# Kernel tuning notes

Hardware: AMD Instinct MI355X
Metric: run time of the kernel (lower is better)

Reference implementation:

```python
import jax, jax.numpy as jnp
import numpy as np

SCENE = (128, 128, 8)      # (X, Y, Z) voxel grid
VOXEL_SIZE = 0.4
DOWNSAMPLE_Z = 2
NUM_HEADS = 8
NUM_POINTS = 4
LN_EPS = 1e-5


def _pix2vox(depth, K, E, voxel_origin):
    # depth [1,H,W]; K [1,3,3]; E [1,4,4]; voxel_origin [1,3]
    B, H, W = depth.shape
    gx, gy = jnp.meshgrid(jnp.arange(W, dtype=depth.dtype), jnp.arange(H, dtype=depth.dtype))
    pix = jnp.stack([gx, gy])                              # [2,H,W] -> (u, v) after flip in torch
    d = depth[:, None]                                     # [B,1,H,W]
    p_x = jnp.concatenate([pix[None] * d, d], 1).reshape(B, 3, -1)
    p_c = jnp.linalg.inv(K) @ p_x                          # camera coords [B,3,HW]
    p_c = jnp.concatenate([p_c, jnp.ones_like(p_c[:, :1])], 1)
    p_w = jnp.linalg.inv(E) @ p_c                          # world coords [B,4,HW]
    p_v = (jnp.swapaxes(p_w[:, :3], 1, 2) - voxel_origin[:, None, :]) / VOXEL_SIZE - 0.5
    p_v = p_v.at[..., 2].set(p_v[..., 2] / DOWNSAMPLE_Z)
    return jnp.trunc(p_v).astype(jnp.int32)               # torch .long() truncates toward 0


def _voxel_mask(p_v):
    X, Y, Z = SCENE
    p = p_v[0]                                             # [HW,3] (batch asserted == 1)
    valid = ((p[:, 0] >= 0) & (p[:, 0] < X) & (p[:, 1] >= 0) & (p[:, 1] < Y)
             & (p[:, 2] >= 0) & (p[:, 2] < Z))
    flat = jnp.where(valid, (p[:, 0] * Y + p[:, 1]) * Z + p[:, 2], 0)
    return jnp.zeros(X * Y * Z, dtype=bool).at[flat].max(valid)


def _ms_deform_attn(q, feats, ref, Wv, bv, Woff, boff, Wattw, battw, Wout, bout):
    # q [N,C]; feats: list of [C,Hl,Wl]; ref [N,2] normalized (shared across levels)
    N, C = q.shape
    hd = C // NUM_HEADS
    shapes = [(f.shape[1], f.shape[2]) for f in feats]
    L = len(feats)
    flat = jnp.concatenate([f.reshape(C, -1).T for f in feats], 0)      # [Lsum, C]
    value = (flat @ Wv.T + bv).reshape(-1, NUM_HEADS, hd)               # [Lsum, h, hd]
    off = (q @ Woff.T + boff).reshape(N, NUM_HEADS, L, NUM_POINTS, 2)
    w = jax.nn.softmax((q @ Wattw.T + battw).reshape(N, NUM_HEADS, L * NUM_POINTS), -1)
    w = w.reshape(N, NUM_HEADS, L, NUM_POINTS)
    normalizer = jnp.array([[wl, hl] for (hl, wl) in shapes], dtype=q.dtype)  # (W,H) per level
    loc = ref[:, None, None, None, :] + off / normalizer[None, None, :, None, :]
    h_idx = jnp.arange(NUM_HEADS)[None, :, None]
    out = jnp.zeros((N, NUM_HEADS, hd), q.dtype)
    start = 0
    for lvl, (Hl, Wl) in enumerate(shapes):
        v = value[start:start + Hl * Wl]                   # [Hl*Wl, h, hd]
        start += Hl * Wl
        # grid_sample bilinear, align_corners=False, zero padding
        x = loc[:, :, lvl, :, 0] * Wl - 0.5                # [N,h,P]
        y = loc[:, :, lvl, :, 1] * Hl - 0.5
        x0 = jnp.floor(x); y0 = jnp.floor(y)
        lx = x - x0; ly = y - y0
        x0i = x0.astype(jnp.int32); y0i = y0.astype(jnp.int32)
        samp = jnp.zeros((N, NUM_HEADS, NUM_POINTS, hd), q.dtype)
        for dy, dx, wgt in ((0, 0, (1 - lx) * (1 - ly)), (0, 1, lx * (1 - ly)),
                            (1, 0, (1 - lx) * ly), (1, 1, lx * ly)):
            xi = x0i + dx; yi = y0i + dy
            ok = (xi >= 0) & (xi < Wl) & (yi >= 0) & (yi < Hl)
            idx = jnp.where(ok, yi * Wl + xi, 0)
            g = v[idx, h_idx]                              # [N,h,P,hd] per-head gather
            samp = samp + g * (wgt * ok)[..., None]
        out = out + jnp.einsum('nhp,nhpd->nhd', w[:, :, lvl], samp)
    return out.reshape(N, C) @ Wout.T + bout


def _forward(scene_embed, feat0, feat1, feat2, depth, K, E, voxel_origin, ref_pix,
             Wv, bv, Woff, boff, Wattw, battw, Wout, bout, ln_g, ln_b):
    X, Y, Z = SCENE
    mask = _voxel_mask(_pix2vox(depth, K, E, voxel_origin))             # [N] bool
    q = scene_embed[0]                                                  # [N,C]
    attn = _ms_deform_attn(q, [feat0[0], feat1[0], feat2[0]], ref_pix[0],
                           Wv, bv, Woff, boff, Wattw, battw, Wout, bout)
    h = q + attn                                                        # residual (MSDeformAttn identity)
    mu = jnp.mean(h, -1, keepdims=True)
    var = jnp.mean((h - mu) ** 2, -1, keepdims=True)
    h = (h - mu) / jnp.sqrt(var + LN_EPS) * ln_g + ln_b                 # post-norm
    out = jnp.where(mask[:, None], h, q)                                # index_fov_back_to_voxels
    return out.T.reshape(1, -1, X, Y, Z)                                # nlc -> nchw [1,C,X,Y,Z]


def setup_inputs() -> dict:
    key = jax.random.key(0)
    ks = jax.random.split(key, 12)
    X, Y, Z = SCENE
    N = X * Y * Z
    C = 128
    H, W = 192, 640
    s = 0.02
    scene_embed = jax.random.normal(ks[0], (1, N, C), jnp.float32)
    feat0 = jax.random.normal(ks[1], (1, C, 48, 160), jnp.float32)
    feat1 = jax.random.normal(ks[2], (1, C, 24, 80), jnp.float32)
    feat2 = jax.random.normal(ks[3], (1, C, 12, 40), jnp.float32)
    depth = jax.random.uniform(ks[4], (1, H, W), jnp.float32, 1.0, 40.0)
    K = jnp.array([[[552.55, 0.0, 320.0], [0.0, 552.55, 96.0], [0.0, 0.0, 1.0]]], jnp.float32)
    E = jnp.eye(4, dtype=jnp.float32)[None]
    voxel_origin = jnp.array([[-25.6, -3.2, 0.0]], jnp.float32)
    ref_pix = jax.random.uniform(ks[5], (1, N, 2), jnp.float32)
    return {
        'scene_embed': scene_embed, 'feat0': feat0, 'feat1': feat1, 'feat2': feat2,
        'depth': depth, 'K': K, 'E': E, 'voxel_origin': voxel_origin, 'ref_pix': ref_pix,
        'Wv': jax.random.normal(ks[6], (C, C), jnp.float32) * s,
        'bv': jnp.zeros((C,), jnp.float32),
        'Woff': jax.random.normal(ks[7], (NUM_HEADS * 3 * NUM_POINTS * 2, C), jnp.float32) * s,
        'boff': jnp.zeros((NUM_HEADS * 3 * NUM_POINTS * 2,), jnp.float32),
        'Wattw': jax.random.normal(ks[8], (NUM_HEADS * 3 * NUM_POINTS, C), jnp.float32) * s,
        'battw': jnp.zeros((NUM_HEADS * 3 * NUM_POINTS,), jnp.float32),
        'Wout': jax.random.normal(ks[9], (C, C), jnp.float32) * s,
        'bout': jnp.zeros((C,), jnp.float32),
        'ln_g': jnp.ones((C,), jnp.float32),
        'ln_b': jnp.zeros((C,), jnp.float32),
    }


def reference(scene_embed, feat0, feat1, feat2, depth, K, E, voxel_origin, ref_pix,
              Wv, bv, Woff, boff, Wattw, battw, Wout, bout, ln_g, ln_b):
    return _forward(scene_embed, feat0, feat1, feat2, depth, K, E, voxel_origin, ref_pix,
                    Wv, bv, Woff, boff, Wattw, battw, Wout, bout, ln_g, ln_b)
```

## Files before the change

### kernel.cpp

```cpp
#include <hip/hip_runtime.h>
#include <hip/hip_bf16.h>
#include <stdint.h>

#define XS 128
#define YS 128
#define ZS 8
#define NQ (XS*YS*ZS)
#define CDIM 128
#define NH 8
#define HD 16
#define DH 192
#define DW 640
#define NPIX (DH*DW)
#define NVPIX 10080

typedef float f32x4 __attribute__((ext_vector_type(4)));
typedef short s16x8 __attribute__((ext_vector_type(8)));

__device__ __forceinline__ float b2f(unsigned short u){
    union { unsigned int i; float f; } v; v.i = ((unsigned int)u) << 16; return v.f;
}
__device__ __forceinline__ unsigned short f2b(float f){
    __hip_bfloat16 h = __float2bfloat16(f);
    return *reinterpret_cast<unsigned short*>(&h);
}
__device__ __forceinline__ float blo(unsigned int u){
    union { unsigned int i; float f; } v; v.i = u << 16; return v.f;
}
__device__ __forceinline__ float bhi(unsigned int u){
    union { unsigned int i; float f; } v; v.i = u & 0xffff0000u; return v.f;
}

__global__ __launch_bounds__(256)
void inv_kernel(const float* __restrict__ K,
                const float* __restrict__ E,
                double* __restrict__ inv_out,
                const float* __restrict__ Woff,
                const float* __restrict__ Wattw,
                const float* __restrict__ Wout,
                unsigned short* __restrict__ Wbf){
    if (blockIdx.x != 0){
        int idx = (blockIdx.x-1)*256 + threadIdx.x;
        if (idx < 24576)      Wbf[idx] = f2b(Woff[idx]);
        else if (idx < 36864) Wbf[idx] = f2b(Wattw[idx-24576]);
        else if (idx < 40960) Wbf[idx] = 0;
        else if (idx < 57344) Wbf[idx] = f2b(Wout[idx-40960]);
        return;
    }
    if (threadIdx.x != 0) return;
    double k[3][3], e[4][4];
    for (int i=0;i<9;i++)  k[i/3][i%3] = (double)K[i];
    for (int i=0;i<16;i++) e[i/4][i%4] = (double)E[i];
    double det = k[0][0]*(k[1][1]*k[2][2]-k[1][2]*k[2][1])
               - k[0][1]*(k[1][0]*k[2][2]-k[1][2]*k[2][0])
               + k[0][2]*(k[1][0]*k[2][1]-k[1][1]*k[2][0]);
    double id = 1.0/det;
    double inv[3][3];
    inv[0][0]=(k[1][1]*k[2][2]-k[1][2]*k[2][1])*id;
    inv[0][1]=(k[0][2]*k[2][1]-k[0][1]*k[2][2])*id;
    inv[0][2]=(k[0][1]*k[1][2]-k[0][2]*k[1][1])*id;
    inv[1][0]=(k[1][2]*k[2][0]-k[1][0]*k[2][2])*id;
    inv[1][1]=(k[0][0]*k[2][2]-k[0][2]*k[2][0])*id;
    inv[1][2]=(k[0][2]*k[1][0]-k[0][0]*k[1][2])*id;
    inv[2][0]=(k[1][0]*k[2][1]-k[1][1]*k[2][0])*id;
    inv[2][1]=(k[0][1]*k[2][0]-k[0][0]*k[2][1])*id;
    inv[2][2]=(k[0][0]*k[1][1]-k[0][1]*k[1][0])*id;
    for (int i=0;i<9;i++) inv_out[i] = inv[i/3][i%3];
    double a[4][8];
    for (int i=0;i<4;i++){ for(int j=0;j<4;j++){ a[i][j]=e[i][j]; a[i][4+j]=(i==j)?1.0:0.0; } }
    for (int c=0;c<4;c++){
        int piv=c; double best=fabs(a[c][c]);
        for (int r=c+1;r<4;r++){ double v=fabs(a[r][c]); if (v>best){best=v;piv=r;} }
        if (piv!=c){ for (int j=0;j<8;j++){ double tmp=a[c][j]; a[c][j]=a[piv][j]; a[piv][j]=tmp; } }
        double pv = 1.0/a[c][c];
        for (int j=0;j<8;j++) a[c][j]*=pv;
        for (int r=0;r<4;r++){
            if (r==c) continue;
            double f=a[r][c];
            for(int j=0;j<8;j++) a[r][j]-=f*a[c][j];
        }
    }
    for (int i=0;i<16;i++) inv_out[9+i] = a[i/4][4 + (i%4)];
}

__global__ __launch_bounds__(256)
void prep2_kernel(int nVal,
                  const float* __restrict__ f0,
                  const float* __restrict__ f1,
                  const float* __restrict__ f2,
                  const float* __restrict__ Wv,
                  const float* __restrict__ bv,
                  unsigned short* __restrict__ value,
                  const float* __restrict__ depth,
                  const double* __restrict__ invm,
                  const float* __restrict__ vorigin,
                  unsigned char* __restrict__ mask){
    __shared__ float fl2[2][CDIM][4];
    const int t = threadIdx.x;
    if ((int)blockIdx.x < nVal){
        const int half = t >> 7, tt = t & 127;
        const int p0 = blockIdx.x*8 + half*4;
        float (*fl)[4] = fl2[half];
        const float* src; int hw, lp;
        if (p0 < 7680)      { src=f0; hw=7680; lp=p0; }
        else if (p0 < 9600) { src=f1; hw=1920; lp=p0-7680; }
        else                { src=f2; hw=480;  lp=p0-9600; }
        float4 v = *(const float4*)(src + tt*hw + lp);
        fl[tt][0]=v.x; fl[tt][1]=v.y; fl[tt][2]=v.z; fl[tt][3]=v.w;
        __syncthreads();
        float bb = bv[tt];
        float acc[4] = {bb,bb,bb,bb};
        const float4* wrow = (const float4*)(Wv + tt*CDIM);
        #pragma unroll 8
        for (int kc=0; kc<32; ++kc){
            float4 w = wrow[kc];
            #pragma unroll
            for (int u=0;u<4;u++){
                float wu = (u==0)?w.x:(u==1)?w.y:(u==2)?w.z:w.w;
                float4 fv = *(const float4*)fl[kc*4+u];
                acc[0] += fv.x*wu; acc[1] += fv.y*wu; acc[2] += fv.z*wu; acc[3] += fv.w*wu;
            }
        }
        const int hh = tt >> 4, cc = tt & 15;
        #pragma unroll
        for (int i=0;i<4;i++)
            value[((size_t)hh*NVPIX + (size_t)(p0+i))*HD + cc] = f2b(acc[i]);
    } else {
        int tid = (blockIdx.x - nVal)*256 + t;
        if (tid >= NPIX) return;
        int gx = tid % DW, gy = tid / DW;
        double d  = (double)depth[tid];
        double X0 = (double)gx * d, X1 = (double)gy * d, X2 = d;
        double c0 = invm[0]*X0 + invm[1]*X1 + invm[2]*X2;
        double c1 = invm[3]*X0 + invm[4]*X1 + invm[5]*X2;
        double c2 = invm[6]*X0 + invm[7]*X1 + invm[8]*X2;
        const double* iE = invm + 9;
        double w0 = iE[0]*c0 + iE[1]*c1 + iE[2]*c2  + iE[3];
        double w1 = iE[4]*c0 + iE[5]*c1 + iE[6]*c2  + iE[7];
        double w2 = iE[8]*c0 + iE[9]*c1 + iE[10]*c2 + iE[11];
        double v0 = (w0-(double)vorigin[0])/0.4 - 0.5;
        double v1 = (w1-(double)vorigin[1])/0.4 - 0.5;
        double v2 = ((w2-(double)vorigin[2])/0.4 - 0.5) / 2.0;
        int xi = (int)v0, yi = (int)v1, zi = (int)v2;
        if (xi>=0 && xi<XS && yi>=0 && yi<YS && zi>=0 && zi<ZS)
            mask[(xi*YS + yi)*ZS + zi] = 1;
    }
}

__global__ __launch_bounds__(256)
void prep_offaw(const float* __restrict__ q_in,
                const unsigned short* __restrict__ Wbf,
                const float* __restrict__ boff,
                const float* __restrict__ battw,
                unsigned short* __restrict__ offawB){
    __shared__ __align__(16) unsigned char smem[54400];
    unsigned short* Ob   = (unsigned short*)smem;
    unsigned char*  qbfB = smem + 36864;
    float*          bias = (float*)(smem + 53248);
    const int t = threadIdx.x;
    const int n0 = blockIdx.x * 64;

    #pragma unroll
    for (int i=0;i<8;i++){
        int idx = t + i*256;
        int row = idx >> 5, c4 = idx & 31;
        float4 qv = ((const float4*)(q_in + (size_t)(n0+row)*CDIM))[c4];
        unsigned int pk0 = (unsigned int)f2b(qv.x) | ((unsigned int)f2b(qv.y)<<16);
        unsigned int pk1 = (unsigned int)f2b(qv.z) | ((unsigned int)f2b(qv.w)<<16);
        unsigned int bo = ((unsigned int)(row*256 + c4*8)) ^ (unsigned int)((row&7)<<4);
        *(unsigned int*)(qbfB + bo)     = pk0;
        *(unsigned int*)(qbfB + bo + 4) = pk1;
    }
    for (int i=t;i<288;i+=256) bias[i] = (i<192)? boff[i] : battw[i-192];
    __syncthreads();

    const int w = t >> 6, lane = t & 63, lr = lane & 15, lg = lane >> 4;
    const int nt0 = w*5;
    f32x4 acc[5][4];
    #pragma unroll
    for (int j=0;j<5;j++)
        #pragma unroll
        for (int qt=0;qt<4;qt++) acc[j][qt] = (f32x4){0.f,0.f,0.f,0.f};

    #pragma unroll
    for (int ks=0; ks<4; ++ks){
        s16x8 bf[4];
        #pragma unroll
        for (int qt=0;qt<4;qt++){
            int qrow = qt*16 + lr;
            unsigned int bo = ((unsigned int)(qrow*256 + ks*64 + lg*16)) ^ (unsigned int)((qrow&7)<<4);
            bf[qt] = *(const s16x8*)(qbfB + bo);
        }
        const unsigned short* wp = Wbf + (size_t)(nt0*16 + lr)*CDIM + ks*32 + lg*8;
        #pragma unroll
        for (int j=0;j<5;++j){
            s16x8 af = *(const s16x8*)(wp + j*16*CDIM);
            #pragma unroll
            for (int qt=0;qt<4;qt++)
                acc[j][qt] = __builtin_amdgcn_mfma_f32_16x16x32_bf16(af, bf[qt], acc[j][qt], 0, 0, 0);
        }
    }

    #pragma unroll
    for (int j=0;j<5;++j){
        int nt = nt0 + j;
        if (nt < 18){
            #pragma unroll
            for (int qt=0;qt<4;qt++){
                int q = qt*16 + lr;
                int base = (q>>3)*2304 + (q&7);
                #pragma unroll
                for (int r=0;r<4;++r){
                    int f = nt*16 + lg*4 + r;
                    Ob[base + f*8] = f2b(acc[j][qt][r] + bias[f]);
                }
            }
        }
    }
    __syncthreads();

    for (int task = t; task < 512; task += 256){
        int q = task >> 3, h = task & 7;
        unsigned short* p = Ob + (q>>3)*2304 + (192 + h*12)*8 + (q&7);
        float e[12]; float m = -1e30f;
        #pragma unroll
        for (int i=0;i<12;i++){ e[i] = b2f(p[i*8]); m = fmaxf(m, e[i]); }
        float s = 0.f;
        #pragma unroll
        for (int i=0;i<12;i++){ e[i] = __expf(e[i]-m); s += e[i]; }
        float is = 1.f/s;
        #pragma unroll
        for (int i=0;i<12;i++) p[i*8] = f2b(e[i]*is);
    }
    __syncthreads();

    {
        const uint4* src = (const uint4*)Ob;
        uint4* dst = (uint4*)(offawB + (size_t)blockIdx.x * 18432);
        for (int idx = t; idx < 2304; idx += 256) dst[idx] = src[idx];
    }
}

__global__ __launch_bounds__(256, 2)
void attn_kernel(const float* __restrict__ q_in,
                 const float* __restrict__ refpix,
                 const unsigned short* __restrict__ offawB,
                 const unsigned short* __restrict__ value,
                 const unsigned short* __restrict__ WoutBf,
                 const float* __restrict__ bout,
                 const float* __restrict__ lng,
                 const float* __restrict__ lnb,
                 const unsigned char* __restrict__ mask,
                 float* __restrict__ dout,
                 int q0g){
    const int n0l = blockIdx.x * 8;
    const int n0g = q0g + n0l;
    const int t = threadIdx.x;
    __shared__ __align__(16) unsigned char smem[25296];
    unsigned short* raw   = (unsigned short*)(smem);
    unsigned char*  descB = smem + 4608;
    float*          out2  = (float*)(smem + 4608);
    unsigned char*  obfB  = smem + 16896;
    float (*q_s)[CDIM]    = (float(*)[CDIM])(smem + 20992);
    float*          rp_s  = (float*)(smem + 25088);
    float*          wredp = (float*)(smem + 25152);
    unsigned char*  mask_s= (unsigned char*)(smem + 25280);

    {
        const unsigned int* src = (const unsigned int*)(offawB + (size_t)(n0l>>3)*2304);
        unsigned int* dst = (unsigned int*)raw;
        #pragma unroll
        for (int i=0;i<5;i++){ int idx = t + i*256; if (idx < 1152) dst[idx] = src[idx]; }
        ((float4*)q_s)[t] = ((const float4*)(q_in + (size_t)n0g*CDIM))[t];
        ((unsigned int*)obfB)[512 + t] = 0;
        ((unsigned int*)obfB)[768 + t] = 0;
        if (t < 16) rp_s[t] = refpix[n0g*2 + t];
        if (t < 8)  mask_s[t] = mask[n0g + t];
    }
    __syncthreads();

    for (int idx = t; idx < 768; idx += 256){
        int q = idx & 7, hp = idx >> 3;
        int lp = hp % 12;
        float fw, fh; int Wl, Hl, st;
        if (lp < 4)      { fw=160.f; fh=48.f; Wl=160; Hl=48; st=0; }
        else if (lp < 8) { fw=80.f;  fh=24.f; Wl=80;  Hl=24; st=7680; }
        else             { fw=40.f;  fh=12.f; Wl=40;  Hl=12; st=9600; }
        float offx = b2f(raw[(hp*2)*8 + q]);
        float offy = b2f(raw[(hp*2+1)*8 + q]);
        float aw   = b2f(raw[(192+hp)*8 + q]);
        float x = rp_s[q*2+0]*fw - 0.5f + offx;
        float y = rp_s[q*2+1]*fh - 0.5f + offy;
        float x0f = floorf(x), y0f = floorf(y);
        float lx = x-x0f, ly = y-y0f;
        int x0 = (int)x0f, y0 = (int)y0f;
        bool x0ok = (x0>=0)&&(x0<Wl), x1ok=(x0+1>=0)&&(x0+1<Wl);
        bool y0ok = (y0>=0)&&(y0<Hl), y1ok=(y0+1>=0)&&(y0+1<Hl);
        float w00 = (x0ok&&y0ok)? (1.f-lx)*(1.f-ly)*aw : 0.f;
        float w01 = (x1ok&&y0ok)? lx*(1.f-ly)*aw       : 0.f;
        float w10 = (x0ok&&y1ok)? (1.f-lx)*ly*aw       : 0.f;
        float w11 = (x1ok&&y1ok)? lx*ly*aw             : 0.f;
        int yc0 = min(max(y0,0),Hl-1), yc1 = min(max(y0+1,0),Hl-1);
        int xc0 = min(max(x0,0),Wl-1), xc1 = min(max(x0+1,0),Wl-1);
        unsigned int rb0 = (unsigned int)(st + yc0*Wl), rb1 = (unsigned int)(st + yc1*Wl);
        uint4 d;
        d.x = (rb0+(unsigned int)xc0) | ((rb0+(unsigned int)xc1)<<16);
        d.y = (rb1+(unsigned int)xc0) | ((rb1+(unsigned int)xc1)<<16);
        d.z = (unsigned int)f2b(w00) | ((unsigned int)f2b(w01)<<16);
        d.w = (unsigned int)f2b(w10) | ((unsigned int)f2b(w11)<<16);
        *(uint4*)(descB + (((unsigned int)(idx ^ ((idx>>5)&7)))<<4)) = d;
    }
    __syncthreads();

    {
        const int cp = t & 7, hs = (t>>3) & 7, qgs = t >> 6;
        const unsigned short* vh = value + ((size_t)hs*NVPIX)*HD + cp*2;
        float av0x=0.f, av0y=0.f, av1x=0.f, av1y=0.f;
        #pragma unroll
        for (int lp=0; lp<12; ++lp){
            #pragma unroll
            for (int qi2=0; qi2<2; ++qi2){
                int idx = (hs*12+lp)*8 + qgs*2 + qi2;
                uint4 d = *(const uint4*)(descB + (((unsigned int)(idx ^ ((idx>>5)&7)))<<4));
                unsigned int p00 = d.x & 0xffffu, p01 = d.x >> 16;
                unsigned int p10 = d.y & 0xffffu, p11 = d.y >> 16;
                unsigned int u00 = *(const unsigned int*)(vh + (p00<<4));
                unsigned int u01 = *(const unsigned int*)(vh + (p01<<4));
                unsigned int u10 = *(const unsigned int*)(vh + (p10<<4));
                unsigned int u11 = *(const unsigned int*)(vh + (p11<<4));
                float w00 = blo(d.z), w01 = bhi(d.z), w10 = blo(d.w), w11 = bhi(d.w);
                float sx = blo(u00)*w00 + blo(u01)*w01 + blo(u10)*w10 + blo(u11)*w11;
                float sy = bhi(u00)*w00 + bhi(u01)*w01 + bhi(u10)*w10 + bhi(u11)*w11;
                if (qi2 == 0){ av0x += sx; av0y += sy; }
                else         { av1x += sx; av1y += sy; }
            }
        }
        const int q0q = qgs*2;
        unsigned int pk0 = (unsigned int)f2b(av0x) | ((unsigned int)f2b(av0y)<<16);
        unsigned int pk1 = (unsigned int)f2b(av1x) | ((unsigned int)f2b(av1y)<<16);
        unsigned int bo0 = (unsigned int)(q0q*256 + hs*32 + cp*4)     ^ (unsigned int)((q0q&7)<<4);
        unsigned int bo1 = (unsigned int)((q0q+1)*256 + hs*32 + cp*4) ^ (unsigned int)(((q0q+1)&7)<<4);
        *(unsigned int*)(obfB + bo0) = pk0;
        *(unsigned int*)(obfB + bo1) = pk1;
    }
    __syncthreads();

    {
        const int w = t >> 6, lane = t & 63, lr = lane & 15, lg = lane >> 4;
        f32x4 a0 = (f32x4){0.f,0.f,0.f,0.f};
        f32x4 a1 = (f32x4){0.f,0.f,0.f,0.f};
        #pragma unroll
        for (int ks=0; ks<4; ++ks){
            unsigned int bo = (unsigned int)(lr*256 + ks*64 + lg*16) ^ (unsigned int)((lr&7)<<4);
            s16x8 bfrag = *(const s16x8*)(obfB + bo);
            const unsigned short* wp = WoutBf + (size_t)(w*32 + lr)*CDIM + ks*32 + lg*8;
            s16x8 af0 = *(const s16x8*)(wp);
            s16x8 af1 = *(const s16x8*)(wp + 16*CDIM);
            a0 = __builtin_amdgcn_mfma_f32_16x16x32_bf16(af0, bfrag, a0, 0, 0, 0);
            a1 = __builtin_amdgcn_mfma_f32_16x16x32_bf16(af1, bfrag, a1, 0, 0, 0);
        }
        if (lr < 8){
            int f0 = w*32 + lg*4;
            float4 b0 = *(const float4*)(bout + f0);
            float4 b1 = *(const float4*)(bout + f0 + 16);
            float4 v0, v1;
            v0.x = a0[0]+b0.x; v0.y = a0[1]+b0.y; v0.z = a0[2]+b0.z; v0.w = a0[3]+b0.w;
            v1.x = a1[0]+b1.x; v1.y = a1[1]+b1.y; v1.z = a1[2]+b1.z; v1.w = a1[3]+b1.w;
            *(float4*)(out2 + lr*CDIM + f0)      = v0;
            *(float4*)(out2 + lr*CDIM + f0 + 16) = v1;
        }
    }
    __syncthreads();

    const int r = t & 127;
    const int qb = t >> 7;
    const int wv = t >> 6;
    float acc[4];
    #pragma unroll
    for (int qi4=0;qi4<4;qi4++) acc[qi4] = out2[(qb*4+qi4)*CDIM + r];

    float hv[4], sred[4];
    #pragma unroll
    for (int qi4=0;qi4<4;qi4++){ hv[qi4] = q_s[qb*4+qi4][r] + acc[qi4]; sred[qi4]=hv[qi4]; }
    #pragma unroll
    for (int off=32; off>0; off>>=1)
        #pragma unroll
        for (int qi4=0;qi4<4;qi4++) sred[qi4] += __shfl_xor(sred[qi4], off, 64);
    if ((t&63)==0){
        #pragma unroll
        for (int qi4=0;qi4<4;qi4++) wredp[0*16 + wv*4 + qi4]=sred[qi4];
    }
    __syncthreads();
    float mu[4], dv[4];
    #pragma unroll
    for (int qi4=0;qi4<4;qi4++){
        mu[qi4] = (wredp[0*16 + (qb*2)*4 + qi4]+wredp[0*16 + (qb*2+1)*4 + qi4]) * (1.f/128.f);
        dv[qi4] = hv[qi4]-mu[qi4];
        sred[qi4] = dv[qi4]*dv[qi4];
    }
    #pragma unroll
    for (int off=32; off>0; off>>=1)
        #pragma unroll
        for (int qi4=0;qi4<4;qi4++) sred[qi4] += __shfl_xor(sred[qi4], off, 64);
    if ((t&63)==0){
        #pragma unroll
        for (int qi4=0;qi4<4;qi4++) wredp[1*16 + wv*4 + qi4]=sred[qi4];
    }
    __syncthreads();

    float res[4];
    const float g = lng[r], b = lnb[r];
    #pragma unroll
    for (int qi4=0;qi4<4;qi4++){
        float var = (wredp[1*16 + (qb*2)*4 + qi4]+wredp[1*16 + (qb*2+1)*4 + qi4]) * (1.f/128.f);
        float nv  = dv[qi4] * __frsqrt_rn(var + 1e-5f) * g + b;
        res[qi4] = mask_s[qb*4+qi4] ? nv : q_s[qb*4+qi4][r];
    }
    float4 o; o.x=res[0]; o.y=res[1]; o.z=res[2]; o.w=res[3];
    *(float4*)(dout + (size_t)r*NQ + n0g + qb*4) = o;
}

extern "C" void kernel_launch(void* const* d_in, const int* in_sizes, int n_in,
                              void* d_out, int out_size, void* d_ws, size_t ws_size,
                              hipStream_t stream){
    const float* scene  = (const float*)d_in[0];
    const float* f0     = (const float*)d_in[1];
    const float* f1     = (const float*)d_in[2];
    const float* f2     = (const float*)d_in[3];
    const float* depth  = (const float*)d_in[4];
    const float* K      = (const float*)d_in[5];
    const float* E      = (const float*)d_in[6];
    const float* vorig  = (const float*)d_in[7];
    const float* refpix = (const float*)d_in[8];
    const float* Wv     = (const float*)d_in[9];
    const float* bv     = (const float*)d_in[10];
    const float* Woff   = (const float*)d_in[11];
    const float* boff   = (const float*)d_in[12];
    const float* Wattw  = (const float*)d_in[13];
    const float* battw  = (const float*)d_in[14];
    const float* Wout   = (const float*)d_in[15];
    const float* bout   = (const float*)d_in[16];
    const float* lng    = (const float*)d_in[17];
    const float* lnb    = (const float*)d_in[18];

    char* ws = (char*)d_ws;
    const size_t FIXED = 512 + 131072 + 2580480 + 114688;
    double*         invm   = (double*)(ws);
    unsigned char*  mask   = (unsigned char*)(ws + 512);
    unsigned short* value  = (unsigned short*)(ws + 512 + 131072);
    unsigned short* Wbf    = (unsigned short*)(ws + 512 + 131072 + 2580480);
    unsigned short* WoutBf = Wbf + 40960;
    unsigned short* offawB = (unsigned short*)(ws + FIXED);

    size_t avail = (ws_size > FIXED) ? (ws_size - FIXED) : 0;
    long long maxq = (long long)(avail / (288*2));
    int chunk = (int)((maxq/64)*64);
    if (chunk > NQ) chunk = NQ;
    if (chunk < 64) chunk = 64;

    hipMemsetAsync(mask, 0, NQ, stream);
    inv_kernel<<<225, 256, 0, stream>>>(K, E, invm, Woff, Wattw, Wout, Wbf);

    int nVal  = NVPIX/8;
    int nMask = (NPIX+255)/256;
    prep2_kernel<<<nVal + nMask, 256, 0, stream>>>(nVal, f0, f1, f2, Wv, bv, value,
                                                   depth, invm, vorig, mask);

    for (int q0 = 0; q0 < NQ; q0 += chunk){
        int len = (NQ - q0 < chunk) ? (NQ - q0) : chunk;
        prep_offaw<<<len/64, 256, 0, stream>>>(scene + (size_t)q0*CDIM,
                                               Wbf, boff, battw, offawB);
        attn_kernel<<<len/8, 256, 0, stream>>>(scene, refpix, offawB, value,
                                               WoutBf, bout, lng, lnb, mask,
                                               (float*)d_out, q0);
    }
}
```

Baseline: 418.9 us.

## Merge value projection and mask build into offset/weight prep launch, batch gather loads

Folds the value projection and voxel-mask blocks into the first chunk of the offset/attention-weight prep kernel, removing one kernel launch and letting those independent blocks run alongside each other. Shared memory for the offset path is cut by aliasing the q staging buffer with the output buffer, guarded by an extra barrier, which may improve occupancy. The attention gather loop is restructured to issue four descriptor loads and sixteen value loads before consuming them, exposing more memory-level parallelism at the cost of extra registers.

```diff
diff --git a/kernel.cpp b/kernel.cpp
--- a/kernel.cpp
+++ b/kernel.cpp
@@ -84,23 +84,115 @@
 }
 
 __global__ __launch_bounds__(256)
-void prep2_kernel(int nVal,
-                  const float* __restrict__ f0,
-                  const float* __restrict__ f1,
-                  const float* __restrict__ f2,
-                  const float* __restrict__ Wv,
-                  const float* __restrict__ bv,
-                  unsigned short* __restrict__ value,
-                  const float* __restrict__ depth,
-                  const double* __restrict__ invm,
-                  const float* __restrict__ vorigin,
-                  unsigned char* __restrict__ mask){
-    __shared__ float fl2[2][CDIM][4];
+void prep_kernel(const float* __restrict__ q_in,
+                 const unsigned short* __restrict__ Wbf,
+                 const float* __restrict__ boff,
+                 const float* __restrict__ battw,
+                 unsigned short* __restrict__ offawB,
+                 int nOff, int nVal,
+                 const float* __restrict__ f0,
+                 const float* __restrict__ f1,
+                 const float* __restrict__ f2,
+                 const float* __restrict__ Wv,
+                 const float* __restrict__ bv,
+                 unsigned short* __restrict__ value,
+                 const float* __restrict__ depth,
+                 const double* __restrict__ invm,
+                 const float* __restrict__ vorigin,
+                 unsigned char* __restrict__ mask){
+    __shared__ __align__(16) unsigned char smem[38016];
     const int t = threadIdx.x;
-    if ((int)blockIdx.x < nVal){
+
+    if ((int)blockIdx.x < nOff){
+        unsigned short* Ob   = (unsigned short*)smem;
+        unsigned char*  qbfB = smem;
+        float*          bias = (float*)(smem + 36864);
+        const int n0 = blockIdx.x * 64;
+
+        #pragma unroll
+        for (int i=0;i<8;i++){
+            int idx = t + i*256;
+            int row = idx >> 5, c4 = idx & 31;
+            float4 qv = ((const float4*)(q_in + (size_t)(n0+row)*CDIM))[c4];
+            unsigned int pk0 = (unsigned int)f2b(qv.x) | ((unsigned int)f2b(qv.y)<<16);
+            unsigned int pk1 = (unsigned int)f2b(qv.z) | ((unsigned int)f2b(qv.w)<<16);
+            unsigned int bo = ((unsigned int)(row*256 + c4*8)) ^ (unsigned int)((row&7)<<4);
+            *(unsigned int*)(qbfB + bo)     = pk0;
+            *(unsigned int*)(qbfB + bo + 4) = pk1;
+        }
+        for (int i=t;i<288;i+=256) bias[i] = (i<192)? boff[i] : battw[i-192];
+        __syncthreads();
+
+        const int w = t >> 6, lane = t & 63, lr = lane & 15, lg = lane >> 4;
+        const int nt0 = w*5;
+        f32x4 acc[5][4];
+        #pragma unroll
+        for (int j=0;j<5;j++)
+            #pragma unroll
+            for (int qt=0;qt<4;qt++) acc[j][qt] = (f32x4){0.f,0.f,0.f,0.f};
+
+        #pragma unroll
+        for (int ks=0; ks<4; ++ks){
+            s16x8 bf[4];
+            #pragma unroll
+            for (int qt=0;qt<4;qt++){
+                int qrow = qt*16 + lr;
+                unsigned int bo = ((unsigned int)(qrow*256 + ks*64 + lg*16)) ^ (unsigned int)((qrow&7)<<4);
+                bf[qt] = *(const s16x8*)(qbfB + bo);
+            }
+            const unsigned short* wp = Wbf + (size_t)(nt0*16 + lr)*CDIM + ks*32 + lg*8;
+            #pragma unroll
+            for (int j=0;j<5;++j){
+                s16x8 af = *(const s16x8*)(wp + j*16*CDIM);
+                #pragma unroll
+                for (int qt=0;qt<4;qt++)
+                    acc[j][qt] = __builtin_amdgcn_mfma_f32_16x16x32_bf16(af, bf[qt], acc[j][qt], 0, 0, 0);
+            }
+        }
+        __syncthreads();
+
+        #pragma unroll
+        for (int j=0;j<5;++j){
+            int nt = nt0 + j;
+            if (nt < 18){
+                #pragma unroll
+                for (int qt=0;qt<4;qt++){
+                    int q = qt*16 + lr;
+                    int base = (q>>3)*2304 + (q&7);
+                    #pragma unroll
+                    for (int r=0;r<4;++r){
+                        int f = nt*16 + lg*4 + r;
+                        Ob[base + f*8] = f2b(acc[j][qt][r] + bias[f]);
+                    }
+                }
+            }
+        }
+        __syncthreads();
+
+        for (int task = t; task < 512; task += 256){
+            int q = task >> 3, h = task & 7;
+            unsigned short* p = Ob + (q>>3)*2304 + (192 + h*12)*8 + (q&7);
+            float e[12]; float m = -1e30f;
+            #pragma unroll
+            for (int i=0;i<12;i++){ e[i] = b2f(p[i*8]); m = fmaxf(m, e[i]); }
+            float s = 0.f;
+            #pragma unroll
+            for (int i=0;i<12;i++){ e[i] = __expf(e[i]-m); s += e[i]; }
+            float is = 1.f/s;
+            #pragma unroll
+            for (int i=0;i<12;i++) p[i*8] = f2b(e[i]*is);
+        }
+        __syncthreads();
+
+        {
+            const uint4* src = (const uint4*)Ob;
+            uint4* dst = (uint4*)(offawB + (size_t)blockIdx.x * 18432);
+            for (int idx = t; idx < 2304; idx += 256) dst[idx] = src[idx];
+        }
+    } else if ((int)blockIdx.x < nOff + nVal){
         const int half = t >> 7, tt = t & 127;
-        const int p0 = blockIdx.x*8 + half*4;
-        float (*fl)[4] = fl2[half];
+        const int p0 = (blockIdx.x - nOff)*8 + half*4;
+        float (*fl)[4] = (float(*)[4])(smem + half*2048);
         const float* src; int hw, lp;
         if (p0 < 7680)      { src=f0; hw=7680; lp=p0; }
         else if (p0 < 9600) { src=f1; hw=1920; lp=p0-7680; }
@@ -126,7 +218,7 @@
         for (int i=0;i<4;i++)
             value[((size_t)hh*NVPIX + (size_t)(p0+i))*HD + cc] = f2b(acc[i]);
     } else {
-        int tid = (blockIdx.x - nVal)*256 + t;
+        int tid = (blockIdx.x - nOff - nVal)*256 + t;
         if (tid >= NPIX) return;
         int gx = tid % DW, gy = tid / DW;
         double d  = (double)depth[tid];
@@ -144,100 +236,6 @@
         int xi = (int)v0, yi = (int)v1, zi = (int)v2;
         if (xi>=0 && xi<XS && yi>=0 && yi<YS && zi>=0 && zi<ZS)
             mask[(xi*YS + yi)*ZS + zi] = 1;
-    }
-}
-
-__global__ __launch_bounds__(256)
-void prep_offaw(const float* __restrict__ q_in,
-                const unsigned short* __restrict__ Wbf,
-                const float* __restrict__ boff,
-                const float* __restrict__ battw,
-                unsigned short* __restrict__ offawB){
-    __shared__ __align__(16) unsigned char smem[54400];
-    unsigned short* Ob   = (unsigned short*)smem;
-    unsigned char*  qbfB = smem + 36864;
-    float*          bias = (float*)(smem + 53248);
-    const int t = threadIdx.x;
-    const int n0 = blockIdx.x * 64;
-
-    #pragma unroll
-    for (int i=0;i<8;i++){
-        int idx = t + i*256;
-        int row = idx >> 5, c4 = idx & 31;
-        float4 qv = ((const float4*)(q_in + (size_t)(n0+row)*CDIM))[c4];
-        unsigned int pk0 = (unsigned int)f2b(qv.x) | ((unsigned int)f2b(qv.y)<<16);
-        unsigned int pk1 = (unsigned int)f2b(qv.z) | ((unsigned int)f2b(qv.w)<<16);
-        unsigned int bo = ((unsigned int)(row*256 + c4*8)) ^ (unsigned int)((row&7)<<4);
-        *(unsigned int*)(qbfB + bo)     = pk0;
-        *(unsigned int*)(qbfB + bo + 4) = pk1;
-    }
-    for (int i=t;i<288;i+=256) bias[i] = (i<192)? boff[i] : battw[i-192];
-    __syncthreads();
-
-    const int w = t >> 6, lane = t & 63, lr = lane & 15, lg = lane >> 4;
-    const int nt0 = w*5;
-    f32x4 acc[5][4];
-    #pragma unroll
-    for (int j=0;j<5;j++)
-        #pragma unroll
-        for (int qt=0;qt<4;qt++) acc[j][qt] = (f32x4){0.f,0.f,0.f,0.f};
-
-    #pragma unroll
-    for (int ks=0; ks<4; ++ks){
-        s16x8 bf[4];
-        #pragma unroll
-        for (int qt=0;qt<4;qt++){
-            int qrow = qt*16 + lr;
-            unsigned int bo = ((unsigned int)(qrow*256 + ks*64 + lg*16)) ^ (unsigned int)((qrow&7)<<4);
-            bf[qt] = *(const s16x8*)(qbfB + bo);
-        }
-        const unsigned short* wp = Wbf + (size_t)(nt0*16 + lr)*CDIM + ks*32 + lg*8;
-        #pragma unroll
-        for (int j=0;j<5;++j){
-            s16x8 af = *(const s16x8*)(wp + j*16*CDIM);
-            #pragma unroll
-            for (int qt=0;qt<4;qt++)
-                acc[j][qt] = __builtin_amdgcn_mfma_f32_16x16x32_bf16(af, bf[qt], acc[j][qt], 0, 0, 0);
-        }
-    }
-
-    #pragma unroll
-    for (int j=0;j<5;++j){
-        int nt = nt0 + j;
-        if (nt < 18){
-            #pragma unroll
-            for (int qt=0;qt<4;qt++){
-                int q = qt*16 + lr;
-                int base = (q>>3)*2304 + (q&7);
-                #pragma unroll
-                for (int r=0;r<4;++r){
-                    int f = nt*16 + lg*4 + r;
-                    Ob[base + f*8] = f2b(acc[j][qt][r] + bias[f]);
-                }
-            }
-        }
-    }
-    __syncthreads();
-
-    for (int task = t; task < 512; task += 256){
-        int q = task >> 3, h = task & 7;
-        unsigned short* p = Ob + (q>>3)*2304 + (192 + h*12)*8 + (q&7);
-        float e[12]; float m = -1e30f;
-        #pragma unroll
-        for (int i=0;i<12;i++){ e[i] = b2f(p[i*8]); m = fmaxf(m, e[i]); }
-        float s = 0.f;
-        #pragma unroll
-        for (int i=0;i<12;i++){ e[i] = __expf(e[i]-m); s += e[i]; }
-        float is = 1.f/s;
-        #pragma unroll
-        for (int i=0;i<12;i++) p[i*8] = f2b(e[i]*is);
-    }
-    __syncthreads();
-
-    {
-        const uint4* src = (const uint4*)Ob;
-        uint4* dst = (uint4*)(offawB + (size_t)blockIdx.x * 18432);
-        for (int idx = t; idx < 2304; idx += 256) dst[idx] = src[idx];
     }
 }
 
@@ -317,21 +315,28 @@
         const unsigned short* vh = value + ((size_t)hs*NVPIX)*HD + cp*2;
         float av0x=0.f, av0y=0.f, av1x=0.f, av1y=0.f;
         #pragma unroll
-        for (int lp=0; lp<12; ++lp){
-            #pragma unroll
-            for (int qi2=0; qi2<2; ++qi2){
+        for (int g=0; g<6; ++g){
+            uint4 d[4];
+            #pragma unroll
+            for (int s=0;s<4;s++){
+                int lp = g*2 + (s>>1), qi2 = s&1;
                 int idx = (hs*12+lp)*8 + qgs*2 + qi2;
-                uint4 d = *(const uint4*)(descB + (((unsigned int)(idx ^ ((idx>>5)&7)))<<4));
-                unsigned int p00 = d.x & 0xffffu, p01 = d.x >> 16;
-                unsigned int p10 = d.y & 0xffffu, p11 = d.y >> 16;
-                unsigned int u00 = *(const unsigned int*)(vh + (p00<<4));
-                unsigned int u01 = *(const unsigned int*)(vh + (p01<<4));
-                unsigned int u10 = *(const unsigned int*)(vh + (p10<<4));
-                unsigned int u11 = *(const unsigned int*)(vh + (p11<<4));
-                float w00 = blo(d.z), w01 = bhi(d.z), w10 = blo(d.w), w11 = bhi(d.w);
-                float sx = blo(u00)*w00 + blo(u01)*w01 + blo(u10)*w10 + blo(u11)*w11;
-                float sy = bhi(u00)*w00 + bhi(u01)*w01 + bhi(u10)*w10 + bhi(u11)*w11;
-                if (qi2 == 0){ av0x += sx; av0y += sy; }
+                d[s] = *(const uint4*)(descB + (((unsigned int)(idx ^ ((idx>>5)&7)))<<4));
+            }
+            unsigned int u[4][4];
+            #pragma unroll
+            for (int s=0;s<4;s++){
+                u[s][0] = *(const unsigned int*)(vh + ((size_t)(d[s].x & 0xffffu)<<4));
+                u[s][1] = *(const unsigned int*)(vh + ((size_t)(d[s].x >> 16)<<4));
+                u[s][2] = *(const unsigned int*)(vh + ((size_t)(d[s].y & 0xffffu)<<4));
+                u[s][3] = *(const unsigned int*)(vh + ((size_t)(d[s].y >> 16)<<4));
+            }
+            #pragma unroll
+            for (int s=0;s<4;s++){
+                float w00 = blo(d[s].z), w01 = bhi(d[s].z), w10 = blo(d[s].w), w11 = bhi(d[s].w);
+                float sx = blo(u[s][0])*w00 + blo(u[s][1])*w01 + blo(u[s][2])*w10 + blo(u[s][3])*w11;
+                float sy = bhi(u[s][0])*w00 + bhi(u[s][1])*w01 + bhi(u[s][2])*w10 + bhi(u[s][3])*w11;
+                if ((s&1)==0){ av0x += sx; av0y += sy; }
                 else         { av1x += sx; av1y += sy; }
             }
         }
@@ -461,15 +466,16 @@
     hipMemsetAsync(mask, 0, NQ, stream);
     inv_kernel<<<225, 256, 0, stream>>>(K, E, invm, Woff, Wattw, Wout, Wbf);
 
-    int nVal  = NVPIX/8;
-    int nMask = (NPIX+255)/256;
-    prep2_kernel<<<nVal + nMask, 256, 0, stream>>>(nVal, f0, f1, f2, Wv, bv, value,
-                                                   depth, invm, vorig, mask);
-
     for (int q0 = 0; q0 < NQ; q0 += chunk){
         int len = (NQ - q0 < chunk) ? (NQ - q0) : chunk;
-        prep_offaw<<<len/64, 256, 0, stream>>>(scene + (size_t)q0*CDIM,
-                                               Wbf, boff, battw, offawB);
+        int nOff  = len/64;
+        int nVal  = (q0 == 0) ? (NVPIX/8) : 0;
+        int nMask = (q0 == 0) ? ((NPIX+255)/256) : 0;
+        prep_kernel<<<nOff + nVal + nMask, 256, 0, stream>>>(
+            scene + (size_t)q0*CDIM, Wbf, boff, battw, offawB,
+            nOff, nVal,
+            f0, f1, f2, Wv, bv, value,
+            depth, invm, vorig, mask);
         attn_kernel<<<len/8, 256, 0, stream>>>(scene, refpix, offawB, value,
                                                WoutBf, bout, lng, lnb, mask,
                                                (float*)d_out, q0);
```

New measurement: 424.0 us. Within noise of the previous version (+1.2%).
